# Kernel tuning notes

Hardware: AMD Instinct MI355X
Metric: run time of the kernel (lower is better)

## Reference

```python
import jax, jax.numpy as jnp
import numpy as np

M, N_ = 2048, 2048
RX, RY = 8, 0
ANGLES = [-10.0, 0.0, 10.0]
BATCH = 2


def _rotate(img, angle):
    # bilinear rotation about center, reshape=False, zeros outside
    # (stands in for scipy.ndimage.rotate(order=2); kernel is an init-time constant)
    if angle % 360 == 0:
        return img.copy()
    h, w = img.shape
    cy, cx = (h - 1) / 2.0, (w - 1) / 2.0
    t = np.deg2rad(angle)
    cs, sn = np.cos(t), np.sin(t)
    ys, xs = np.meshgrid(np.arange(h, dtype=np.float64), np.arange(w, dtype=np.float64), indexing='ij')
    y0, x0 = ys - cy, xs - cx
    sy = cs * y0 + sn * x0 + cy
    sx = -sn * y0 + cs * x0 + cx
    y0i = np.floor(sy).astype(np.int64)
    x0i = np.floor(sx).astype(np.int64)
    wy = sy - y0i
    wx = sx - x0i
    out = np.zeros_like(img, dtype=np.float64)
    for dy in (0, 1):
        for dx in (0, 1):
            yy = y0i + dy
            xx = x0i + dx
            valid = (yy >= 0) & (yy < h) & (xx >= 0) & (xx < w)
            wgt = (wy if dy else 1.0 - wy) * (wx if dx else 1.0 - wx)
            vals = np.where(valid, img[np.clip(yy, 0, h - 1), np.clip(xx, 0, w - 1)], 0.0)
            out += wgt * vals
    return out


def _build_kernels(rx, ry, angles):
    # mirrors GuidedFilter.__init__ kernel construction
    kl = []
    for A in angles:
        kern = np.zeros((rx * 4 + 1, rx * 4 + 1), dtype=np.float64)
        if ry == 0:
            kern[:, rx * 2] = 1.0
        else:
            kern[:, rx * 2 - ry:rx * 2 + ry + 1] = 1.0
        kern = _rotate(kern, A)[rx:3 * rx + 1, rx:3 * rx + 1]
        r = int((kern.sum(1) != 0).sum()) // 2 * 2
        c = int((kern.sum(0) != 0).sum()) // 2 * 2
        kl.append(kern[rx - r // 2: rx + r // 2 + 1, rx - c // 2: rx + c // 2 + 1][None, None])
    C = max(k.shape[-2] for k in kl)
    R = max(k.shape[-1] for k in kl)
    out = np.zeros((len(angles), 1, C, R), dtype=np.float32)
    for i, k in enumerate(kl):
        oh = (C - k.shape[-2]) // 2
        ow = (R - k.shape[-1]) // 2
        out[i, :, oh:oh + k.shape[-2], ow:ow + k.shape[-1]] = k
    return out


def _boxfilter(x, k, pc, pr):
    # torch: conv2d(F.pad(x, (pr, pr, pc, pc)), k) == explicit-padding cross-correlation
    return jax.lax.conv_general_dilated(
        x, k, window_strides=(1, 1),
        padding=((pc, pc), (pr, pr)),
        dimension_numbers=('NCHW', 'OIHW', 'NCHW'))


def setup_inputs() -> dict:
    key = jax.random.key(0)
    k1, k2 = jax.random.split(key)
    X = jax.random.uniform(k1, (BATCH, 1, M, N_), dtype=jnp.float32)
    y = jax.random.uniform(k2, (BATCH, 1, M, N_), dtype=jnp.float32)
    kernel = jnp.asarray(_build_kernels(RX, RY, ANGLES))  # (A,1,kh,kw)
    pc, pr = kernel.shape[-2] // 2, kernel.shape[-1] // 2
    ones = jnp.ones((1, 1, M, N_), jnp.float32)
    N_norm = jnp.concatenate(
        [_boxfilter(ones, kernel[i:i + 1], pc, pr) for i in range(len(ANGLES))], axis=0)  # (A,1,M,N)
    return {"X": X, "y": y, "kernel": kernel, "N_norm": N_norm}


def reference(X, y, kernel, N_norm):
    pc, pr = kernel.shape[-2] // 2, kernel.shape[-1] // 2
    n_angle = kernel.shape[0]
    for i in range(n_angle):  # small fixed loop over angles (structurally distinct kernels)
        k = kernel[i:i + 1]            # (1,1,kh,kw)
        Ni = N_norm[i][None]           # (1,1,M,N) broadcasts over batch
        mean_y = _boxfilter(y, k, pc, pr) / Ni
        mean_x = _boxfilter(X, k, pc, pr) / Ni
        X = X + (mean_y - mean_x)
    return X
```

## Files before the change

### kernel.cpp

```cpp
#include <hip/hip_runtime.h>
#include <hip/hip_fp16.h>
#include <math.h>
#include <string.h>
#include <stdint.h>

#define HH 2048
#define WW 2048
#define INBX 32
#define INBY 32
#define NINT1 ((INBX - 2) * (INBY - 2))
#define NBND 496
#define TOT1 (NINT1 + NBND)

#define H0 42
#define H1 34
#define G0 40
#define G1 38

struct W3 {
  float wA[17][5]; float wC[17][5]; float wB[17];
  float knA, knB, knC;
  unsigned uA[17], uC[17], uA8b, uC8b;
};
struct Wts { float w[17][5]; float knorm; };

__host__ __device__ constexpr int js_fn(int a, int i) {
  return (a == 1) ? 2
       : (a == 2) ? ((i < 3) ? 0 : (i < 9) ? 1 : (i < 14) ? 2 : 3)
                  : ((i < 3) ? 3 : (i < 8) ? 2 : (i < 14) ? 1 : 0);
}
__host__ __device__ constexpr int nt_fn(int a, int i) {
  return (a == 1) ? 1 : (i == 8) ? 3 : 2;
}

__device__ __forceinline__ float fastrcp(float x) {
#if __has_builtin(__builtin_amdgcn_rcpf)
  return __builtin_amdgcn_rcpf(x);
#else
  return 1.0f / x;
#endif
}

__device__ __forceinline__ __half2 pack2(float a, float b) {
  return __float22half2_rn(make_float2(a, b));
}

typedef _Float16 h2vec __attribute__((ext_vector_type(2)));

__device__ __forceinline__ float fdot2h(unsigned win, unsigned wgt, float acc) {
#if __has_builtin(__builtin_amdgcn_fdot2)
  return __builtin_amdgcn_fdot2(__builtin_bit_cast(h2vec, win),
                                __builtin_bit_cast(h2vec, wgt), acc, false);
#else
  const __half2 ha = __builtin_bit_cast(__half2, win);
  const __half2 hb = __builtin_bit_cast(__half2, wgt);
  const float2 fa = __half22float2(ha), fb = __half22float2(hb);
  return fmaf(fa.y, fb.y, fmaf(fa.x, fb.x, acc));
#endif
}

__global__ __launch_bounds__(256, 4)
void fused_all(const float* __restrict__ Xg, const float* __restrict__ Yg,
               const float* __restrict__ Nn, float* __restrict__ Out, W3 w)
{
  __shared__ __half2 ldsh[8160];

  const int bid = blockIdx.x, nwg = gridDim.x;
  const int wg = ((nwg & 7) == 0) ? ((bid & 7) * (nwg >> 3) + (bid >> 3)) : bid;
  const int bz = wg / TOT1;
  const int t0 = wg - bz * TOT1;
  const int tid = threadIdx.x;
  const size_t img = (size_t)bz * ((size_t)HH * WW);

  if (t0 < NINT1) {
    __half2* buf0h = ldsh;
    __half2* buf1h = ldsh + 4704;
    __half2* buf2h = buf0h;

    const int bx = 1 + t0 / (INBY - 2);
    const int by = 1 + t0 % (INBY - 2);
    const int x0 = bx * 64, y0 = by * 64;

#pragma unroll
    for (int s = 0; s < 9; ++s) {
      const int idx = s * 256 + tid;
      if (idx < 112 * 20) {
        const int r = idx / 20, c4 = idx - r * 20;
        const size_t g = img + (size_t)(y0 - 24 + r) * WW + (x0 - 8 + c4 * 4);
        const float4 xv = *(const float4*)(Xg + g);
        const float4 yv = *(const float4*)(Yg + g);
        buf0h[r * H0 + c4 * 2]     = pack2(yv.x - xv.x, yv.y - xv.y);
        buf0h[r * H0 + c4 * 2 + 1] = pack2(yv.z - xv.z, yv.w - xv.w);
      }
    }
    __syncthreads();

#pragma unroll 1
    for (int tt = tid; tt < 408; tt += 256) {
      const int rg = tt / 17, cg = tt - rg * 17;
      const int r0 = rg * 4, c0 = cg * 4;
      float acc[4][4] = {};
#pragma unroll
      for (int rr = 0; rr < 20; ++rr) {
        const unsigned* lp = (const unsigned*)&buf0h[(r0 + rr) * H0 + (c0 >> 1)];
        const uint2 qa = *(const uint2*)(lp + 2);
        const uint2 qb = *(const uint2*)(lp + 4);
        unsigned p[7];
        p[0] = qa.x;  p[2] = qa.y;  p[4] = qb.x;  p[6] = qb.y;
        p[1] = __builtin_amdgcn_alignbit(qa.y, qa.x, 16);
        p[3] = __builtin_amdgcn_alignbit(qb.x, qa.y, 16);
        p[5] = __builtin_amdgcn_alignbit(qb.y, qb.x, 16);
#pragma unroll
        for (int t = 0; t < 4; ++t) {
          const int i = rr - t;
          if (i >= 0 && i <= 16) {
            const int js = js_fn(0, i);
            if (i != 8) {
              const unsigned w2 = w.uA[i];
#pragma unroll
              for (int c = 0; c < 4; ++c)
                acc[t][c] = fdot2h(p[js + c], w2, acc[t][c]);
            } else {
              const unsigned w2a = w.uA[8], w2b = w.uA8b;
#pragma unroll
              for (int c = 0; c < 4; ++c) {
                acc[t][c] = fdot2h(p[1 + c], w2a, acc[t][c]);
                acc[t][c] = fdot2h(p[3 + c], w2b, acc[t][c]);
              }
            }
          }
        }
      }
#pragma unroll
      for (int t = 0; t < 4; ++t) {
        const unsigned* cp = (const unsigned*)&buf0h[(r0 + t + 8) * H0 + (c0 >> 1)];
        const float2 c01 = __half22float2(__builtin_bit_cast(__half2, cp[3]));
        const float2 c23 = __half22float2(__builtin_bit_cast(__half2, cp[4]));
        buf1h[(r0 + t) * H1 + (c0 >> 1)]     = pack2(c01.x - acc[t][0], c01.y - acc[t][1]);
        buf1h[(r0 + t) * H1 + (c0 >> 1) + 1] = pack2(c23.x - acc[t][2], c23.y - acc[t][3]);
      }
    }
    __syncthreads();

#pragma unroll 1
    for (int tt = tid; tt < 340; tt += 256) {
      const int rg = tt / 17, cg = tt - rg * 17;
      const int r0 = rg * 4, c0 = cg * 4;
      float acc[4][4] = {};
#pragma unroll
      for (int rr = 0; rr < 20; ++rr) {
        const __half2* lp = &buf1h[(r0 + rr) * H1 + (c0 >> 1)];
        const float2 a = __half22float2(lp[0]);
        const float2 b = __half22float2(lp[1]);
        const float win[4] = {a.x, a.y, b.x, b.y};
#pragma unroll
        for (int t = 0; t < 4; ++t) {
          const int i = rr - t;
          if (i >= 0 && i <= 16) {
            const float wv = w.wB[i];
            acc[t][0] = fmaf(wv, win[0], acc[t][0]);
            acc[t][1] = fmaf(wv, win[1], acc[t][1]);
            acc[t][2] = fmaf(wv, win[2], acc[t][2]);
            acc[t][3] = fmaf(wv, win[3], acc[t][3]);
          }
        }
      }
#pragma unroll
      for (int t = 0; t < 4; ++t) {
        const __half2* cp = &buf1h[(r0 + t + 8) * H1 + (c0 >> 1)];
        const float2 ca = __half22float2(cp[0]);
        const float2 cb = __half22float2(cp[1]);
        buf2h[(r0 + t) * H1 + (c0 >> 1)]     = pack2(ca.x - acc[t][0], ca.y - acc[t][1]);
        buf2h[(r0 + t) * H1 + (c0 >> 1) + 1] = pack2(cb.x - acc[t][2], cb.y - acc[t][3]);
      }
    }
    __syncthreads();

    {
      const int tg = tid >> 4, tc = tid & 15;
      const int r0 = tg * 4, c0 = tc * 4;
      float acc[4][4] = {};
#pragma unroll
      for (int rr = 0; rr < 20; ++rr) {
        const unsigned* lp = (const unsigned*)&buf2h[(r0 + rr) * H1 + (c0 >> 1)];
        const uint2 qa = *(const uint2*)(lp);
        const uint2 qb = *(const uint2*)(lp + 2);
        unsigned p[7];
        p[0] = qa.x;  p[2] = qa.y;  p[4] = qb.x;  p[6] = qb.y;
        p[1] = __builtin_amdgcn_alignbit(qa.y, qa.x, 16);
        p[3] = __builtin_amdgcn_alignbit(qb.x, qa.y, 16);
        p[5] = __builtin_amdgcn_alignbit(qb.y, qb.x, 16);
#pragma unroll
        for (int t = 0; t < 4; ++t) {
          const int i = rr - t;
          if (i >= 0 && i <= 16) {
            const int js = js_fn(2, i);
            if (i != 8) {
              const unsigned w2 = w.uC[i];
#pragma unroll
              for (int c = 0; c < 4; ++c)
                acc[t][c] = fdot2h(p[js + c], w2, acc[t][c]);
            } else {
#pragma unroll
              for (int c = 0; c < 4; ++c) {
                acc[t][c] = fdot2h(p[1 + c], w.uC[8], acc[t][c]);
                acc[t][c] = fdot2h(p[3 + c], w.uC8b, acc[t][c]);
              }
            }
          }
        }
      }
#pragma unroll
      for (int t = 0; t < 4; ++t) {
        const __half2* cp = &buf2h[(r0 + t + 8) * H1 + (c0 >> 1)];
        const float2 ca = __half22float2(cp[1]);
        const float2 cb = __half22float2(cp[2]);
        const int gy = y0 + r0 + t, gx = x0 + c0;
        const float4 yv = *(const float4*)(Yg + img + (size_t)gy * WW + gx);
        *(float4*)(Out + img + (size_t)gy * WW + gx) = make_float4(
            yv.x - ca.x + acc[t][0], yv.y - ca.y + acc[t][1],
            yv.z - cb.x + acc[t][2], yv.w - cb.y + acc[t][3]);
      }
    }
  } else {
    __half2* buf0h = ldsh;
    __half2* buf1h = ldsh + 2560;
    __half2* buf2h = buf0h;

    const int u = t0 - NINT1;
    int x0, y0;
    if (u < 128)      { y0 = (u >> 5) * 16;                x0 = (u & 31) * 64; }
    else if (u < 256) { const int v = u - 128;
                        y0 = 1984 + ((v >> 5) * 16);       x0 = (v & 31) * 64; }
    else              { const int v = u - 256;
                        const int side = v & 1, row = v >> 1;
                        y0 = 64 + row * 16;
                        x0 = side ? 1984 : 0; }

    const float* N0 = Nn;
    const float* N1 = Nn + (size_t)HH * WW;
    const float* N2 = Nn + 2 * (size_t)HH * WW;

#pragma unroll
    for (int s = 0; s < 5; ++s) {
      const int idx = s * 256 + tid;
      const int r = idx / 20, c4 = idx - r * 20;
      const int gy = y0 - 24 + r;
      const int gx = x0 - 8 + c4 * 4;
      float4 v = make_float4(0.f, 0.f, 0.f, 0.f);
      if (gy >= 0 && gy < HH) {
        const float* xr = Xg + img + (size_t)gy * WW;
        const float* yr = Yg + img + (size_t)gy * WW;
        if (gx >= 0 && gx + 4 <= WW) {
          const float4 xv = *(const float4*)(xr + gx);
          const float4 yv = *(const float4*)(yr + gx);
          v = make_float4(yv.x - xv.x, yv.y - xv.y, yv.z - xv.z, yv.w - xv.w);
        } else {
          float tv[4] = {0.f, 0.f, 0.f, 0.f};
#pragma unroll
          for (int e = 0; e < 4; ++e) {
            const int gxe = gx + e;
            if (gxe >= 0 && gxe < WW) tv[e] = yr[gxe] - xr[gxe];
          }
          v = make_float4(tv[0], tv[1], tv[2], tv[3]);
        }
      }
      buf0h[r * G0 + c4 * 2]     = pack2(v.x, v.y);
      buf0h[r * G0 + c4 * 2 + 1] = pack2(v.z, v.w);
    }
    __syncthreads();

    if (tid < 216) {
      const int rg = tid / 18, cg = tid - rg * 18;
      const int r0 = rg * 4, c0 = cg * 4;
      float acc[4][4] = {};
#pragma unroll
      for (int rr = 0; rr < 20; ++rr) {
        const __half2* lp = &buf0h[(r0 + rr) * G0 + (c0 >> 1)];
        const float2 p0 = __half22float2(lp[1]);
        const float2 p1 = __half22float2(lp[2]);
        const float2 p2 = __half22float2(lp[3]);
        const float2 p3 = __half22float2(lp[4]);
        const float win[8] = {p0.x, p0.y, p1.x, p1.y, p2.x, p2.y, p3.x, p3.y};
#pragma unroll
        for (int t = 0; t < 4; ++t) {
          const int i = rr - t;
          if (i >= 0 && i <= 16) {
            const int js = js_fn(0, i), nt = nt_fn(0, i);
#pragma unroll
            for (int jj = 0; jj < nt; ++jj) {
              const float wv = w.wA[i][js + jj];
#pragma unroll
              for (int c = 0; c < 4; ++c)
                acc[t][c] = fmaf(wv, win[c + js + jj], acc[t][c]);
            }
          }
        }
      }
#pragma unroll
      for (int t = 0; t < 4; ++t) {
        const int gy = y0 - 16 + r0 + t;
        const bool rok = (gy >= 0) && (gy < HH);
        const __half2* cp = &buf0h[(r0 + t + 8) * G0 + (c0 >> 1)];
        const float2 c01 = __half22float2(cp[2]);
        const float2 c23 = __half22float2(cp[3]);
        const float cenv[4] = {c01.x, c01.y, c23.x, c23.y};
        float d[4];
#pragma unroll
        for (int c = 0; c < 4; ++c) {
          const int gxc = x0 - 4 + c0 + c;
          const bool ok = rok && (gxc >= 0) && (gxc < WW);
          float r = 0.0f;
          if (ok) {
            const float n = N0[(size_t)gy * WW + gxc];
            r = cenv[c] - acc[t][c] * w.knA * fastrcp(n);
          }
          d[c] = r;
        }
        buf1h[(r0 + t) * G1 + (c0 >> 1)]     = pack2(d[0], d[1]);
        buf1h[(r0 + t) * G1 + (c0 >> 1) + 1] = pack2(d[2], d[3]);
      }
    }
    __syncthreads();

    if (tid < 136) {
      const int rg = tid / 17, cg = tid - rg * 17;
      const int r0 = rg * 4, c0 = cg * 4;
      float acc[4][4] = {};
#pragma unroll
      for (int rr = 0; rr < 20; ++rr) {
        const __half2* lp = &buf1h[(r0 + rr) * G1 + (c0 >> 1)];
        const float2 a = __half22float2(lp[1]);
        const float2 b = __half22float2(lp[2]);
        const float win[4] = {a.x, a.y, b.x, b.y};
#pragma unroll
        for (int t = 0; t < 4; ++t) {
          const int i = rr - t;
          if (i >= 0 && i <= 16) {
            const float wv = w.wB[i];
            acc[t][0] = fmaf(wv, win[0], acc[t][0]);
            acc[t][1] = fmaf(wv, win[1], acc[t][1]);
            acc[t][2] = fmaf(wv, win[2], acc[t][2]);
            acc[t][3] = fmaf(wv, win[3], acc[t][3]);
          }
        }
      }
#pragma unroll
      for (int t = 0; t < 4; ++t) {
        const int gy = y0 - 8 + r0 + t;
        const bool rok = (gy >= 0) && (gy < HH);
        const __half2* cp = &buf1h[(r0 + t + 8) * G1 + (c0 >> 1)];
        const float2 ca = __half22float2(cp[1]);
        const float2 cb = __half22float2(cp[2]);
        const float cenv[4] = {ca.x, ca.y, cb.x, cb.y};
        float d[4];
#pragma unroll
        for (int c = 0; c < 4; ++c) {
          const int gxc = x0 - 2 + c0 + c;
          const bool ok = rok && (gxc >= 0) && (gxc < WW);
          float r = 0.0f;
          if (ok) {
            const float n = N1[(size_t)gy * WW + gxc];
            r = cenv[c] - acc[t][c] * w.knB * fastrcp(n);
          }
          d[c] = r;
        }
        buf2h[(r0 + t) * G1 + (c0 >> 1)]     = pack2(d[0], d[1]);
        buf2h[(r0 + t) * G1 + (c0 >> 1) + 1] = pack2(d[2], d[3]);
      }
    }
    __syncthreads();

    if (tid < 64) {
      const int rg = tid >> 4, tc = tid & 15;
      const int r0 = rg * 4, c0 = tc * 4;
      float acc[4][4] = {};
#pragma unroll
      for (int rr = 0; rr < 20; ++rr) {
        const __half2* lp = &buf2h[(r0 + rr) * G1 + (c0 >> 1)];
        const float2 p0 = __half22float2(lp[0]);
        const float2 p1 = __half22float2(lp[1]);
        const float2 p2 = __half22float2(lp[2]);
        const float2 p3 = __half22float2(lp[3]);
        const float win[8] = {p0.x, p0.y, p1.x, p1.y, p2.x, p2.y, p3.x, p3.y};
#pragma unroll
        for (int t = 0; t < 4; ++t) {
          const int i = rr - t;
          if (i >= 0 && i <= 16) {
            const int js = js_fn(2, i), nt = nt_fn(2, i);
#pragma unroll
            for (int jj = 0; jj < nt; ++jj) {
              const float wv = w.wC[i][js + jj];
#pragma unroll
              for (int c = 0; c < 4; ++c)
                acc[t][c] = fmaf(wv, win[c + js + jj], acc[t][c]);
            }
          }
        }
      }
#pragma unroll
      for (int t = 0; t < 4; ++t) {
        const __half2* cp = &buf2h[(r0 + t + 8) * G1 + (c0 >> 1)];
        const float2 ca = __half22float2(cp[1]);
        const float2 cb = __half22float2(cp[2]);
        const int gy = y0 + r0 + t, gx = x0 + c0;
        const float4 yv = *(const float4*)(Yg + img + (size_t)gy * WW + gx);
        const float4 nv = *(const float4*)(N2 + (size_t)gy * WW + gx);
        *(float4*)(Out + img + (size_t)gy * WW + gx) = make_float4(
            yv.x - ca.x + acc[t][0] * w.knC * fastrcp(nv.x),
            yv.y - ca.y + acc[t][1] * w.knC * fastrcp(nv.y),
            yv.z - cb.x + acc[t][2] * w.knC * fastrcp(nv.z),
            yv.w - cb.y + acc[t][3] * w.knC * fastrcp(nv.w));
      }
    }
  }
}

__global__ __launch_bounds__(256)
void diff_kernel(const float* __restrict__ X, const float* __restrict__ Y,
                 float* __restrict__ D, int n4)
{
  const int stride = gridDim.x * 256;
  for (int i = blockIdx.x * 256 + threadIdx.x; i < n4; i += stride) {
    const float4 x = ((const float4*)X)[i];
    const float4 y = ((const float4*)Y)[i];
    ((float4*)D)[i] = make_float4(y.x - x.x, y.y - x.y, y.z - x.z, y.w - x.w);
  }
}

template <int MODE>
__global__ __launch_bounds__(256, 3)
void conv_dense(const float* __restrict__ P0, const float* __restrict__ P1,
                const float* __restrict__ Nrm, float* __restrict__ Out, Wts wts)
{
  constexpr int DTSC = 128, DTSR = 32;
  constexpr int LSTR = 148, LCW = 36, XOFF = 8, CH = 48 * LCW;
  __shared__ float lds[48 * 148];
  const int bx = blockIdx.x, by = blockIdx.y, bz = blockIdx.z;
  const int tid = threadIdx.x;
  const int x0 = bx * DTSC, y0 = by * DTSR;
  const size_t img = (size_t)bz * ((size_t)HH * WW);
  const float* A = P0 + img;
#pragma unroll
  for (int s = 0; s < (CH + 255) / 256; ++s) {
    const int idx = s * 256 + tid;
    if (idx < CH) {
      const int r = idx / LCW, c4 = idx - r * LCW;
      const int gy = y0 - 8 + r, gx = x0 - XOFF + c4 * 4;
      float4 v = make_float4(0.f, 0.f, 0.f, 0.f);
      if (gy >= 0 && gy < HH) {
        const float* ar = A + (size_t)gy * WW;
        if (gx >= 0 && gx + 4 <= WW) v = *(const float4*)(ar + gx);
        else {
          float tv[4] = {0.f, 0.f, 0.f, 0.f};
#pragma unroll
          for (int e = 0; e < 4; ++e) {
            const int gxe = gx + e;
            if (gxe >= 0 && gxe < WW) tv[e] = ar[gxe];
          }
          v = make_float4(tv[0], tv[1], tv[2], tv[3]);
        }
      }
      *(float4*)&lds[r * LSTR + c4 * 4] = v;
    }
  }
  __syncthreads();
  const int tc = tid & 31, tg = tid >> 5, lc = tc * 4;
  float acc[4][4] = {};
#pragma unroll
  for (int rr = 0; rr < 20; ++rr) {
    const float* lp = &lds[(tg * 4 + rr) * LSTR];
    const float4 w0 = *(const float4*)(lp + 4 + lc);
    const float4 w1 = *(const float4*)(lp + 8 + lc);
    const float4 w2 = *(const float4*)(lp + 12 + lc);
    const float win[8] = {w0.z, w0.w, w1.x, w1.y, w1.z, w1.w, w2.x, w2.y};
#pragma unroll
    for (int t = 0; t < 4; ++t) {
      const int i = rr - t;
      if (i >= 0 && i <= 16) {
#pragma unroll
        for (int jj = 0; jj < 5; ++jj) {
          const float wv = wts.w[i][jj];
#pragma unroll
          for (int c = 0; c < 4; ++c)
            acc[t][c] = fmaf(wv, win[c + jj], acc[t][c]);
        }
      }
    }
  }
  float* Ob = Out + img;
  const int gx = x0 + lc;
  const float kn = wts.knorm;
#pragma unroll
  for (int t = 0; t < 4; ++t) {
    const int yo = y0 + tg * 4 + t;
    const float4 cv = *(const float4*)&lds[(tg * 4 + t + 8) * LSTR + XOFF + lc];
    const float4 nv = *(const float4*)(Nrm + (size_t)yo * WW + gx);
    const float a0 = acc[t][0] * kn * fastrcp(nv.x);
    const float a1 = acc[t][1] * kn * fastrcp(nv.y);
    const float a2 = acc[t][2] * kn * fastrcp(nv.z);
    const float a3 = acc[t][3] * kn * fastrcp(nv.w);
    float4 o;
    if (MODE == 2) {
      const float4 yv = *(const float4*)(P1 + img + (size_t)yo * WW + gx);
      o = make_float4(yv.x - cv.x + a0, yv.y - cv.y + a1,
                      yv.z - cv.z + a2, yv.w - cv.w + a3);
    } else {
      o = make_float4(cv.x - a0, cv.y - a1, cv.z - a2, cv.w - a3);
    }
    *(float4*)(Ob + (size_t)yo * WW + gx) = o;
  }
}

static void rotate33(const double* src, double* dst, double ang_deg) {
  const int n = 33;
  const double t = ang_deg * 3.14159265358979323846 / 180.0;
  const double cs = cos(t), sn = sin(t);
  for (int y = 0; y < n; ++y) {
    for (int x = 0; x < n; ++x) {
      const double y0 = y - 16.0, x0 = x - 16.0;
      const double sy = cs * y0 + sn * x0 + 16.0;
      const double sx = -sn * y0 + cs * x0 + 16.0;
      const double fy = floor(sy), fx = floor(sx);
      const int y0i = (int)fy, x0i = (int)fx;
      const double wy = sy - fy, wx = sx - fx;
      double o = 0.0;
      for (int dy = 0; dy < 2; ++dy)
        for (int dx = 0; dx < 2; ++dx) {
          const int yy = y0i + dy, xx = x0i + dx;
          if (yy < 0 || yy >= n || xx < 0 || xx >= n) continue;
          const double wgt = (dy ? wy : 1.0 - wy) * (dx ? wx : 1.0 - wx);
          o += wgt * src[yy * n + xx];
        }
      dst[y * n + x] = o;
    }
  }
}

static void build_K(float K[3][17][5]) {
  const double angs[3] = {-10.0, 0.0, 10.0};
  double base[33 * 33], rot[33 * 33];
  for (int i = 0; i < 33 * 33; ++i) base[i] = 0.0;
  for (int y = 0; y < 33; ++y) base[y * 33 + 16] = 1.0;
  for (int a = 0; a < 3; ++a) {
    if (a == 1) memcpy(rot, base, sizeof(rot));
    else        rotate33(base, rot, angs[a]);
    double k17[17][17];
    for (int y = 0; y < 17; ++y)
      for (int x = 0; x < 17; ++x) k17[y][x] = rot[(y + 8) * 33 + (x + 8)];
    int r = 0, c = 0;
    for (int y = 0; y < 17; ++y) { bool nz = false; for (int x = 0; x < 17; ++x) if (k17[y][x] != 0.0) nz = true; r += nz; }
    for (int x = 0; x < 17; ++x) { bool nz = false; for (int y = 0; y < 17; ++y) if (k17[y][x] != 0.0) nz = true; c += nz; }
    r = r / 2 * 2; c = c / 2 * 2;
    const int kh = r + 1, kw = c + 1;
    for (int y = 0; y < 17; ++y)
      for (int x = 0; x < 5; ++x) K[a][y][x] = 0.0f;
    if (kh <= 17 && kw <= 5) {
      const int oh = (17 - kh) / 2, ow = (5 - kw) / 2;
      for (int y = 0; y < kh; ++y)
        for (int x = 0; x < kw; ++x)
          K[a][oh + y][ow + x] = (float)k17[8 - r / 2 + y][8 - c / 2 + x];
    }
  }
}

static int pick_mode(int a, const float K[17][5]) {
  for (int i = 0; i < 17; ++i) {
    const int js = js_fn(a, i), nt = nt_fn(a, i);
    for (int j = 0; j < 5; ++j)
      if ((j < js || j >= js + nt) && K[i][j] != 0.0f) return 1;
  }
  return 0;
}

static unsigned short f2h(float f) {
  union { float f; uint32_t u; } v; v.f = f;
  const uint32_t u = v.u;
  const uint32_t s = (u >> 16) & 0x8000u;
  const int32_t  e = (int32_t)((u >> 23) & 0xffu) - 127 + 15;
  const uint32_t m = u & 0x7fffffu;
  if ((u & 0x7fffffffu) == 0) return (unsigned short)s;
  if (e >= 31) return (unsigned short)(s | 0x7bffu);
  if (e <= 0)  return (unsigned short)s;
  uint32_t h = s | ((uint32_t)e << 10) | (m >> 13);
  const uint32_t rem = m & 0x1fffu;
  if (rem > 0x1000u || (rem == 0x1000u && (h & 1u))) h++;
  return (unsigned short)h;
}
static unsigned pack_h2f(float a, float b) {
  return (unsigned)f2h(a) | ((unsigned)f2h(b) << 16);
}

extern "C" void kernel_launch(void* const* d_in, const int* in_sizes, int n_in,
                              void* d_out, int out_size, void* d_ws, size_t ws_size,
                              hipStream_t stream) {
  const float* X  = (const float*)d_in[0];
  const float* Y  = (const float*)d_in[1];
  const float* Nn = (const float*)d_in[3];
  float* out = (float*)d_out;
  float* tmp = (float*)d_ws;
  const size_t HW = (size_t)HH * WW;
  const int B = in_sizes[0] / (int)HW;

  float K[3][17][5];
  build_K(K);
  double ks[3];
  for (int a = 0; a < 3; ++a) {
    ks[a] = 0.0;
    for (int i = 0; i < 17; ++i)
      for (int j = 0; j < 5; ++j) ks[a] += K[a][i][j];
  }
  const int dense = pick_mode(0, K[0]) | pick_mode(1, K[1]) | pick_mode(2, K[2]);

  if (!dense) {
    W3 w;
    for (int i = 0; i < 17; ++i)
      for (int j = 0; j < 5; ++j) {
        w.wA[i][j] = (float)(K[0][i][j] / ks[0]);
        w.wC[i][j] = (float)(K[2][i][j] / ks[2]);
      }
    for (int i = 0; i < 17; ++i) w.wB[i] = (float)(K[1][i][2] / ks[1]);
    w.knA = (float)ks[0]; w.knB = (float)ks[1]; w.knC = (float)ks[2];
    for (int i = 0; i < 17; ++i) {
      const int ja = js_fn(0, i);
      const int jc = js_fn(2, i);
      w.uA[i] = pack_h2f(w.wA[i][ja], w.wA[i][ja + 1]);
      w.uC[i] = pack_h2f(w.wC[i][jc], w.wC[i][jc + 1]);
    }
    w.uA8b = pack_h2f(w.wA[8][js_fn(0, 8) + 2], 0.0f);
    w.uC8b = pack_h2f(w.wC[8][js_fn(2, 8) + 2], 0.0f);

    fused_all<<<dim3(TOT1 * B), dim3(256), 0, stream>>>(X, Y, Nn, out, w);
  } else {
    Wts w[3];
    for (int a = 0; a < 3; ++a) {
      for (int i = 0; i < 17; ++i)
        for (int j = 0; j < 5; ++j) w[a].w[i][j] = (float)(K[a][i][j] / ks[a]);
      w[a].knorm = (float)ks[a];
    }
    const int n4 = (int)(B * HW / 4);
    const int dg = (n4 + 255) / 256;
    diff_kernel<<<dim3(dg > 8192 ? 8192 : dg), dim3(256), 0, stream>>>(X, Y, tmp, n4);
    dim3 g(16, 64, B), blk(256);
    conv_dense<1><<<g, blk, 0, stream>>>(tmp, nullptr, Nn,          out, w[0]);
    conv_dense<1><<<g, blk, 0, stream>>>(out, nullptr, Nn + HW,     tmp, w[1]);
    conv_dense<2><<<g, blk, 0, stream>>>(tmp, Y,       Nn + 2 * HW, out, w[2]);
  }
}
```

Baseline: 56.16 us.

## Double workgroup size to 512 threads and remap per-thread work in fused kernel

Launches the fused kernel with 512 threads per workgroup instead of 256. The load and the first two stage loops now take one tile per thread instead of looping. The final stage now computes 4x2 outputs per thread instead of 4x4. The intent is to raise parallelism per tile and cut the serial tail where a second pass covered only part of the work. The cost is that launch_bounds(512,4) limits registers per thread, and the boundary path, which still assumes 256 threads in parts not shown, may leave threads idle or behave inconsistently.

Result: slower. 77.09 us (+37.3%).

```diff
diff --git a/kernel.cpp b/kernel.cpp
--- a/kernel.cpp
+++ b/kernel.cpp
@@ -59,7 +59,7 @@
 #endif
 }
 
-__global__ __launch_bounds__(256, 4)
+__global__ __launch_bounds__(512, 4)
 void fused_all(const float* __restrict__ Xg, const float* __restrict__ Yg,
                const float* __restrict__ Nn, float* __restrict__ Out, W3 w)
 {
@@ -82,8 +82,8 @@
     const int x0 = bx * 64, y0 = by * 64;
 
 #pragma unroll
-    for (int s = 0; s < 9; ++s) {
-      const int idx = s * 256 + tid;
+    for (int s = 0; s < 5; ++s) {
+      const int idx = s * 512 + tid;
       if (idx < 112 * 20) {
         const int r = idx / 20, c4 = idx - r * 20;
         const size_t g = img + (size_t)(y0 - 24 + r) * WW + (x0 - 8 + c4 * 4);
@@ -95,9 +95,8 @@
     }
     __syncthreads();
 
-#pragma unroll 1
-    for (int tt = tid; tt < 408; tt += 256) {
-      const int rg = tt / 17, cg = tt - rg * 17;
+    if (tid < 408) {
+      const int rg = tid / 17, cg = tid - rg * 17;
       const int r0 = rg * 4, c0 = cg * 4;
       float acc[4][4] = {};
 #pragma unroll
@@ -142,9 +141,8 @@
     }
     __syncthreads();
 
-#pragma unroll 1
-    for (int tt = tid; tt < 340; tt += 256) {
-      const int rg = tt / 17, cg = tt - rg * 17;
+    if (tid < 340) {
+      const int rg = tid / 17, cg = tid - rg * 17;
       const int r0 = rg * 4, c0 = cg * 4;
       float acc[4][4] = {};
 #pragma unroll
@@ -177,19 +175,18 @@
     __syncthreads();
 
     {
-      const int tg = tid >> 4, tc = tid & 15;
-      const int r0 = tg * 4, c0 = tc * 4;
-      float acc[4][4] = {};
+      const int tg = tid >> 5, tc = tid & 31;
+      const int r0 = tg * 4;
+      float acc[4][2] = {};
 #pragma unroll
       for (int rr = 0; rr < 20; ++rr) {
-        const unsigned* lp = (const unsigned*)&buf2h[(r0 + rr) * H1 + (c0 >> 1)];
+        const unsigned* lp = (const unsigned*)&buf2h[(r0 + rr) * H1 + tc];
         const uint2 qa = *(const uint2*)(lp);
-        const uint2 qb = *(const uint2*)(lp + 2);
-        unsigned p[7];
-        p[0] = qa.x;  p[2] = qa.y;  p[4] = qb.x;  p[6] = qb.y;
+        const unsigned d2 = lp[2];
+        unsigned p[5];
+        p[0] = qa.x;  p[2] = qa.y;  p[4] = d2;
         p[1] = __builtin_amdgcn_alignbit(qa.y, qa.x, 16);
-        p[3] = __builtin_amdgcn_alignbit(qb.x, qa.y, 16);
-        p[5] = __builtin_amdgcn_alignbit(qb.y, qb.x, 16);
+        p[3] = __builtin_amdgcn_alignbit(d2, qa.y, 16);
 #pragma unroll
         for (int t = 0; t < 4; ++t) {
           const int i = rr - t;
@@ -198,11 +195,11 @@
             if (i != 8) {
               const unsigned w2 = w.uC[i];
 #pragma unroll
-              for (int c = 0; c < 4; ++c)
+              for (int c = 0; c < 2; ++c)
                 acc[t][c] = fdot2h(p[js + c], w2, acc[t][c]);
             } else {
 #pragma unroll
-              for (int c = 0; c < 4; ++c) {
+              for (int c = 0; c < 2; ++c) {
                 acc[t][c] = fdot2h(p[1 + c], w.uC[8], acc[t][c]);
                 acc[t][c] = fdot2h(p[3 + c], w.uC8b, acc[t][c]);
               }
@@ -212,14 +209,11 @@
       }
 #pragma unroll
       for (int t = 0; t < 4; ++t) {
-        const __half2* cp = &buf2h[(r0 + t + 8) * H1 + (c0 >> 1)];
-        const float2 ca = __half22float2(cp[1]);
-        const float2 cb = __half22float2(cp[2]);
-        const int gy = y0 + r0 + t, gx = x0 + c0;
-        const float4 yv = *(const float4*)(Yg + img + (size_t)gy * WW + gx);
-        *(float4*)(Out + img + (size_t)gy * WW + gx) = make_float4(
-            yv.x - ca.x + acc[t][0], yv.y - ca.y + acc[t][1],
-            yv.z - cb.x + acc[t][2], yv.w - cb.y + acc[t][3]);
+        const float2 cv = __half22float2(buf2h[(r0 + t + 8) * H1 + tc + 1]);
+        const int gy = y0 + r0 + t, gx = x0 + tc * 2;
+        const float2 yv = *(const float2*)(Yg + img + (size_t)gy * WW + gx);
+        *(float2*)(Out + img + (size_t)gy * WW + gx) =
+            make_float2(yv.x - cv.x + acc[t][0], yv.y - cv.y + acc[t][1]);
       }
     }
   } else {
@@ -242,31 +236,33 @@
     const float* N2 = Nn + 2 * (size_t)HH * WW;
 
 #pragma unroll
-    for (int s = 0; s < 5; ++s) {
-      const int idx = s * 256 + tid;
-      const int r = idx / 20, c4 = idx - r * 20;
-      const int gy = y0 - 24 + r;
-      const int gx = x0 - 8 + c4 * 4;
-      float4 v = make_float4(0.f, 0.f, 0.f, 0.f);
-      if (gy >= 0 && gy < HH) {
-        const float* xr = Xg + img + (size_t)gy * WW;
-        const float* yr = Yg + img + (size_t)gy * WW;
-        if (gx >= 0 && gx + 4 <= WW) {
-          const float4 xv = *(const float4*)(xr + gx);
-          const float4 yv = *(const float4*)(yr + gx);
-          v = make_float4(yv.x - xv.x, yv.y - xv.y, yv.z - xv.z, yv.w - xv.w);
-        } else {
-          float tv[4] = {0.f, 0.f, 0.f, 0.f};
-#pragma unroll
-          for (int e = 0; e < 4; ++e) {
-            const int gxe = gx + e;
-            if (gxe >= 0 && gxe < WW) tv[e] = yr[gxe] - xr[gxe];
-          }
-          v = make_float4(tv[0], tv[1], tv[2], tv[3]);
-        }
-      }
-      buf0h[r * G0 + c4 * 2]     = pack2(v.x, v.y);
-      buf0h[r * G0 + c4 * 2 + 1] = pack2(v.z, v.w);
+    for (int s = 0; s < 3; ++s) {
+      const int idx = s * 512 + tid;
+      if (idx < 1280) {
+        const int r = idx / 20, c4 = idx - r * 20;
+        const int gy = y0 - 24 + r;
+        const int gx = x0 - 8 + c4 * 4;
+        float4 v = make_float4(0.f, 0.f, 0.f, 0.f);
+        if (gy >= 0 && gy < HH) {
+          const float* xr = Xg + img + (size_t)gy * WW;
+          const float* yr = Yg + img + (size_t)gy * WW;
+          if (gx >= 0 && gx + 4 <= WW) {
+            const float4 xv = *(const float4*)(xr + gx);
+            const float4 yv = *(const float4*)(yr + gx);
+            v = make_float4(yv.x - xv.x, yv.y - xv.y, yv.z - xv.z, yv.w - xv.w);
+          } else {
+            float tv[4] = {0.f, 0.f, 0.f, 0.f};
+#pragma unroll
+            for (int e = 0; e < 4; ++e) {
+              const int gxe = gx + e;
+              if (gxe >= 0 && gxe < WW) tv[e] = yr[gxe] - xr[gxe];
+            }
+            v = make_float4(tv[0], tv[1], tv[2], tv[3]);
+          }
+        }
+        buf0h[r * G0 + c4 * 2]     = pack2(v.x, v.y);
+        buf0h[r * G0 + c4 * 2 + 1] = pack2(v.z, v.w);
+      }
     }
     __syncthreads();
 
@@ -630,7 +626,7 @@
     w.uA8b = pack_h2f(w.wA[8][js_fn(0, 8) + 2], 0.0f);
     w.uC8b = pack_h2f(w.wC[8][js_fn(2, 8) + 2], 0.0f);
 
-    fused_all<<<dim3(TOT1 * B), dim3(256), 0, stream>>>(X, Y, Nn, out, w);
+    fused_all<<<dim3(TOT1 * B), dim3(512), 0, stream>>>(X, Y, Nn, out, w);
   } else {
     Wts w[3];
     for (int a = 0; a < 3; ++a) {
```
